# Optimization experiments

Measured on AMD Instinct MI355X. Metric: run time of the kernel, lower is better.

## Reference

```python
import jax, jax.numpy as jnp
import numpy as np

N = 50000; E = 800000; F_IN = 128; H = 16; G = 256
DIMS = [F_IN, H, 2 * H, 4 * H, 4 * H, 8 * H]
EPS = 1e-5


def setup_inputs() -> dict:
    key = jax.random.key(0)
    ks = iter(jax.random.split(key, 40))
    inp = {}
    inp["x"] = jax.random.normal(next(ks), (N, F_IN), dtype=jnp.float32)
    inp["edge_index"] = jax.random.randint(next(ks), (2, E), 0, N, dtype=jnp.int32)
    inp["edge_weight"] = jax.random.uniform(next(ks), (E,), dtype=jnp.float32)
    inp["batch"] = jnp.sort(jax.random.randint(next(ks), (N,), 0, G, dtype=jnp.int32))
    for i in range(5):
        din, dout = DIMS[i], DIMS[i + 1]
        inp[f"W{i+1}"] = jax.random.normal(next(ks), (din, dout), dtype=jnp.float32) / np.sqrt(din).astype(np.float32)
        inp[f"b{i+1}"] = jnp.zeros((dout,), jnp.float32)
        inp[f"g{i+1}"] = jnp.ones((dout,), jnp.float32)
        inp[f"bt{i+1}"] = jnp.zeros((dout,), jnp.float32)
    inp["fc1_w"] = jax.random.normal(next(ks), (8 * H, 4 * H), dtype=jnp.float32) / np.sqrt(8 * H).astype(np.float32)
    inp["fc1_b"] = jnp.zeros((4 * H,), jnp.float32)
    inp["fc2_w"] = jax.random.normal(next(ks), (4 * H, 1), dtype=jnp.float32) / np.sqrt(4 * H).astype(np.float32)
    inp["fc2_b"] = jnp.zeros((1,), jnp.float32)
    return inp


def _gcn_norm(edge_index, edge_weight, n):
    # PyG GCNConv: add self-loops (weight 1), symmetric deg^-1/2 normalization.
    loop = jnp.arange(n, dtype=edge_index.dtype)
    row = jnp.concatenate([edge_index[0], loop])  # source
    col = jnp.concatenate([edge_index[1], loop])  # target
    w = jnp.concatenate([edge_weight, jnp.ones((n,), edge_weight.dtype)])
    deg = jax.ops.segment_sum(w, col, num_segments=n)
    dis = jnp.where(deg > 0, jax.lax.rsqrt(jnp.maximum(deg, 1e-12)), 0.0)
    return row, col, dis[row] * w * dis[col]


def _bn(h, g, b):
    # BatchNorm1d, training-mode batch statistics (biased variance, eps=1e-5)
    mu = h.mean(0)
    v = h.var(0)
    return g * (h - mu) * jax.lax.rsqrt(v + EPS) + b


def reference(x, edge_index, edge_weight, batch,
              W1, b1, g1, bt1, W2, b2, g2, bt2, W3, b3, g3, bt3,
              W4, b4, g4, bt4, W5, b5, g5, bt5,
              fc1_w, fc1_b, fc2_w, fc2_b):
    n = x.shape[0]
    row, col, norm = _gcn_norm(edge_index, edge_weight, n)

    def conv(h, W, b):
        m = h @ W                                   # [N, dout] dense transform
        agg = jax.ops.segment_sum(m[row] * norm[:, None], col, num_segments=n)
        return agg + b

    h = _bn(jax.nn.relu(conv(x, W1, b1)), g1, bt1)
    h = _bn(jax.nn.relu(conv(h, W2, b2)), g2, bt2)
    h = _bn(jax.nn.relu(conv(h, W3, b3)), g3, bt3)
    h = jax.nn.relu(_bn(conv(h, W4, b4), g4, bt4))   # layer4: conv->bn->relu
    h = _bn(conv(h, W5, b5), g5, bt5)                # layer5: conv->bn
    pooled = jax.ops.segment_sum(h, batch, num_segments=G)  # global_add_pool -> [G, 8H]
    p = jax.nn.relu(pooled)
    p = jax.nn.relu(p @ fc1_w + fc1_b)
    # dropout is identity in eval mode
    return (p @ fc2_w + fc2_b).reshape(-1)          # [G]
```

## Files before the change

kernel.cpp:

```cpp
#include <hip/hip_runtime.h>
#include <hip/hip_fp16.h>
#include <stdint.h>

#define NN 50000
#define NE 800000
#define NG 256
#define NBUCKET 16
#define PARTSZ (NBUCKET * 256)

#define NBKT 391
#define ABLK 391
#define ASLICE 2048
#define BCAP 2560

__device__ __forceinline__ float bf2f(unsigned short u) {
    return __uint_as_float(((unsigned)u) << 16);
}
__device__ __forceinline__ unsigned short f2bf(float f) {
    unsigned b = __float_as_uint(f);
    return (unsigned short)((b + 0x7FFF + ((b >> 16) & 1)) >> 16);
}
__device__ __forceinline__ unsigned short f2h(float f) {
    __half h = __float2half(f);
    return *(unsigned short*)&h;
}
__device__ __forceinline__ float h2f(unsigned short u) {
    __half h = *(__half*)&u;
    return __half2float(h);
}

#define AFF4(u, sc, sh) { u.x = fmaxf(sc.x*u.x+sh.x,0.f); u.y = fmaxf(sc.y*u.y+sh.y,0.f); \
                          u.z = fmaxf(sc.z*u.z+sh.z,0.f); u.w = fmaxf(sc.w*u.w+sh.w,0.f); }

__device__ __forceinline__ void scan_totals(const int* __restrict__ totals,
                                            int* __restrict__ sbase, int tid) {
    if (tid < 64) {
        const int C = (NBKT + 63) / 64;
        int tv[C];
        int s = 0;
        int i0 = tid * C;
#pragma unroll
        for (int j = 0; j < C; ++j) {
            int idx = i0 + j;
            int x = (idx < NBKT) ? totals[idx] : 0;
            tv[j] = x; s += x;
        }
        int inc = s;
        for (int off = 1; off < 64; off <<= 1) {
            int t2 = __shfl_up(inc, off, 64);
            if (tid >= off) inc += t2;
        }
        int run = inc - s;
#pragma unroll
        for (int j = 0; j < C; ++j) {
            int idx = i0 + j;
            if (idx < NBKT) sbase[idx] = run;
            run += tv[j];
        }
        if (tid == 63) sbase[NBKT] = run;
    }
}

__global__ void kA1(const int* __restrict__ col, int* __restrict__ bb, float* part, int e) {
    __shared__ int cnt[NBKT];
    for (int j = threadIdx.x; j < NBKT; j += 256) cnt[j] = 0;
    for (int i = blockIdx.x * 256 + threadIdx.x; i < 5 * PARTSZ; i += ABLK * 256) part[i] = 0.f;
    __syncthreads();
    int start = blockIdx.x * ASLICE;
    int end = min(start + ASLICE, e);
    for (int i = start + threadIdx.x; i < end; i += 256)
        atomicAdd(&cnt[col[i] >> 7], 1);
    __syncthreads();
    for (int j = threadIdx.x; j < NBKT; j += 256) bb[blockIdx.x * NBKT + j] = cnt[j];
}

__global__ void kA2a(int* __restrict__ bb, int* __restrict__ totals) {
    __shared__ int v[ABLK];
    int k = blockIdx.x;
    int tid = threadIdx.x;
    for (int b = tid; b < ABLK; b += 256) v[b] = bb[b * NBKT + k];
    __syncthreads();
    if (tid < 64) {
        const int C = (ABLK + 63) / 64;
        int tv[C];
        int s = 0;
        int i0 = tid * C;
#pragma unroll
        for (int j = 0; j < C; ++j) {
            int idx = i0 + j;
            int x = (idx < ABLK) ? v[idx] : 0;
            tv[j] = x; s += x;
        }
        int inc = s;
        for (int off = 1; off < 64; off <<= 1) {
            int t2 = __shfl_up(inc, off, 64);
            if (tid >= off) inc += t2;
        }
        int run = inc - s;
#pragma unroll
        for (int j = 0; j < C; ++j) {
            int idx = i0 + j;
            if (idx < ABLK) v[idx] = run;
            run += tv[j];
        }
        if (tid == 63) totals[k] = run;
    }
    __syncthreads();
    for (int b = tid; b < ABLK; b += 256) bb[b * NBKT + k] = v[b];
}

__global__ void kA3g(const int* __restrict__ row, const int* __restrict__ col,
                     const float* __restrict__ ew, const int* __restrict__ bb,
                     const int* __restrict__ totals, int2* __restrict__ staging,
                     const float* __restrict__ x, const float* __restrict__ W0,
                     float* __restrict__ m1, int e, int n) {
    __shared__ int cur[NBKT];
    __shared__ int sbase[NBKT + 1];
    __shared__ float Wl[128 * 16];
    int tid = threadIdx.x;
    if ((int)blockIdx.x < ABLK) {
        scan_totals(totals, sbase, tid);
        __syncthreads();
        for (int j = tid; j < NBKT; j += 256)
            cur[j] = sbase[j] + bb[blockIdx.x * NBKT + j];
        __syncthreads();
        int start = blockIdx.x * ASLICE;
        int end = min(start + ASLICE, e);
        for (int i = start + tid; i < end; i += 256) {
            int c = col[i];
            int p = atomicAdd(&cur[c >> 7], 1);
            staging[p] = make_int2(row[i] | ((c & 127) << 16), __float_as_int(ew[i]));
        }
        return;
    }
    int bid = (int)blockIdx.x - ABLK;
    for (int i = tid; i < 128 * 16 / 4; i += 256)
        ((float4*)Wl)[i] = ((const float4*)W0)[i];
    __syncthreads();
    int jq = tid % 4, group = tid / 4;
    int node0 = (bid * 64 + group) * 2;
    const float4* h4 = (const float4*)x;
    int hb[2]; bool val[2];
#pragma unroll
    for (int i = 0; i < 2; ++i) {
        int nd = node0 + i;
        val[i] = nd < n;
        hb[i] = (val[i] ? nd : n - 1) * 32;
    }
    float4 acc[2];
    acc[0] = {0,0,0,0}; acc[1] = {0,0,0,0};
#pragma unroll 4
    for (int k4 = 0; k4 < 32; ++k4) {
        const float* wb = &Wl[(k4 * 4) * 16 + jq * 4];
        float4 w0 = *(const float4*)(wb);
        float4 w1 = *(const float4*)(wb + 16);
// ... 1 lines not shown
        float4 w3 = *(const float4*)(wb + 48);
#pragma unroll
        for (int i = 0; i < 2; ++i) {
            float4 hv = h4[hb[i] + k4];
            acc[i].x += hv.x*w0.x + hv.y*w1.x + hv.z*w2.x + hv.w*w3.x;
            acc[i].y += hv.x*w0.y + hv.y*w1.y + hv.z*w2.y + hv.w*w3.y;
            acc[i].z += hv.x*w0.z + hv.y*w1.z + hv.z*w2.z + hv.w*w3.z;
            acc[i].w += hv.x*w0.w + hv.y*w1.w + hv.z*w2.w + hv.w*w3.w;
        }
    }
#pragma unroll
    for (int i = 0; i < 2; ++i)
        if (val[i]) ((float4*)m1)[(node0 + i) * 4 + jq] = acc[i];
}

__global__ void __launch_bounds__(256) kB(const int* __restrict__ totals,
                                          const int2* __restrict__ staging,
                                          unsigned int* __restrict__ csr, int* __restrict__ ptr,
                                          float* __restrict__ dis, int n) {
    __shared__ int2 st[BCAP];
    __shared__ unsigned int outb[BCAP];
    __shared__ int hist[129];
    __shared__ int cur[128];
    __shared__ int sbase[NBKT + 1];
    int k = blockIdx.x, t = threadIdx.x;
    scan_totals(totals, sbase, t);
    if (t < 129) hist[t] = 0;
    __syncthreads();
    int base = sbase[k], cnt = sbase[k + 1] - sbase[k];
    int node0 = k << 7;
    int ncov = min(128, n - node0);
    if (cnt <= BCAP) {
        for (int i = t; i < cnt; i += 256) {
            int2 v = staging[base + i];
            st[i] = v;
            atomicAdd(&hist[v.x >> 16], 1);
        }
        __syncthreads();
        if (t == 0) {
            int run = 0;
            for (int j = 0; j < 128; ++j) { int h = hist[j]; hist[j] = run; run += h; }
            hist[128] = run;
        }
        __syncthreads();
        if (t < 128) cur[t] = hist[t];
        if (t < ncov) ptr[node0 + t] = base + hist[t];
        __syncthreads();
        for (int i = t; i < cnt; i += 256) {
            int2 v = st[i];
            int j = v.x >> 16;
            int p = atomicAdd(&cur[j], 1);
            outb[p] = (unsigned)(v.x & 0xFFFF) | ((unsigned)f2h(__int_as_float(v.y)) << 16);
        }
        __syncthreads();
        for (int i = t; i < cnt; i += 256) csr[base + i] = outb[i];
        if (t < ncov) {
            float s = 1.f;
            int a = hist[t], b2 = hist[t + 1];
            for (int p = a; p < b2; ++p) s += h2f((unsigned short)(outb[p] >> 16));
            dis[node0 + t] = rsqrtf(s);
        }
    } else {
        for (int i = t; i < cnt; i += 256) atomicAdd(&hist[staging[base + i].x >> 16], 1);
        __syncthreads();
        if (t == 0) {
            int run = 0;
            for (int j = 0; j < 128; ++j) { int h = hist[j]; hist[j] = run; run += h; }
            hist[128] = run;
        }
        __syncthreads();
        if (t < 128) cur[t] = hist[t];
        if (t < ncov) ptr[node0 + t] = base + hist[t];
        __syncthreads();
        for (int i = t; i < cnt; i += 256) {
            int2 v = staging[base + i];
            int j = v.x >> 16;
            int p = atomicAdd(&cur[j], 1);
            csr[base + p] = (unsigned)(v.x & 0xFFFF) | ((unsigned)f2h(__int_as_float(v.y)) << 16);
        }
        __threadfence_block();
        __syncthreads();
        if (t < ncov) {
            float s = 1.f;
            int a = hist[t], b2 = hist[t + 1];
            for (int p = a; p < b2; ++p) s += h2f((unsigned short)(csr[base + p] >> 16));
            dis[node0 + t] = rsqrtf(s);
        }
    }
    if (k == gridDim.x - 1 && t == 0) ptr[n] = sbase[NBKT];
}

__global__ void k_l1gather(const float* __restrict__ src, const int* __restrict__ ptr,
                           unsigned int* __restrict__ csr, const float* __restrict__ dis,
                           const float* __restrict__ bias, float* __restrict__ partOut,
                           float* __restrict__ out, int n) {
    __shared__ float ls[16], lq[16];
    int tid = threadIdx.x;
    if (tid < 16) { ls[tid] = 0.f; lq[tid] = 0.f; }
    __syncthreads();
    int t = blockIdx.x * 256 + tid;
    int node = t >> 2;
    int l4 = t & 3;
    bool valid = node < n;
    int nc = valid ? node : n - 1;
    const float4* s4 = (const float4*)src;
    float dc = dis[nc];
    float w0 = dc * dc;
    float4 v = s4[nc * 4 + l4];
    float4 acc = { w0 * v.x, w0 * v.y, w0 * v.z, w0 * v.w };
// ... 42 lines not shown
        s0 += __shfl_down(s0, off, 64); s1 += __shfl_down(s1, off, 64);
        s2 += __shfl_down(s2, off, 64); s3 += __shfl_down(s3, off, 64);
        q0 += __shfl_down(q0, off, 64); q1 += __shfl_down(q1, off, 64);
        q2 += __shfl_down(q2, off, 64); q3 += __shfl_down(q3, off, 64);
    }
    int lane = tid & 63;
    if (lane < 4) {
        atomicAdd(&ls[4*lane+0], s0); atomicAdd(&ls[4*lane+1], s1);
        atomicAdd(&ls[4*lane+2], s2); atomicAdd(&ls[4*lane+3], s3);
        atomicAdd(&lq[4*lane+0], q0); atomicAdd(&lq[4*lane+1], q1);
        atomicAdd(&lq[4*lane+2], q2); atomicAdd(&lq[4*lane+3], q3);
    }
    __syncthreads();
    int bkt = (blockIdx.x & (NBUCKET - 1)) * 256;
    if (tid < 16) {
        atomicAdd(&partOut[bkt + tid], ls[tid]);
        atomicAdd(&partOut[bkt + 128 + tid], lq[tid]);
    }
}

template <int D, int BF16>
__device__ __forceinline__ float4 load_row(const void* src, int node, int l4) {
    if (BF16) {
        const unsigned short* sb = (const unsigned short*)src;
        ushort4 r = *(const ushort4*)(sb + (size_t)node * D + (l4 << 2));
        float4 f;
        f.x = bf2f(r.x); f.y = bf2f(r.y); f.z = bf2f(r.z); f.w = bf2f(r.w);
        return f;
    } else {
        const float4* s4 = (const float4*)src;
        return s4[(size_t)node * (D / 4) + l4];
    }
}

template <int D>
__device__ __forceinline__ void ldrow16(const unsigned short* __restrict__ src, int node, int l8,
                                        float4& a, float4& b) {
    uint4 r = *(const uint4*)(src + (size_t)node * D + (l8 << 3));
    a.x = bf2f((unsigned short)(r.x)); a.y = bf2f((unsigned short)(r.x >> 16));
    a.z = bf2f((unsigned short)(r.y)); a.w = bf2f((unsigned short)(r.y >> 16));
    b.x = bf2f((unsigned short)(r.z)); b.y = bf2f((unsigned short)(r.z >> 16));
    b.z = bf2f((unsigned short)(r.w)); b.w = bf2f((unsigned short)(r.w >> 16));
}

template <int DIN, int DOUT, int EP, int POSTAFF, int PREAFF, int RELU,
          int BF16IN, int BF16OUT, int NPB>
__global__ void __launch_bounds__(256) k_fused(
        const void* __restrict__ src, const int* __restrict__ ptr,
        const unsigned int* __restrict__ csr, const float* __restrict__ dis,
        const float* __restrict__ partIn, const float* __restrict__ gmv,
        const float* __restrict__ btv, const float* __restrict__ W,
        const float* __restrict__ bias, float* __restrict__ partOut,
        void* __restrict__ out, int n) {
    const int TPN1 = DIN / 4, LPN = TPN1 * EP, GN1 = 256 / LPN;
    const int TPN2 = DOUT / 4, G2 = 256 / TPN2;
    const int HS = DIN + 4;
    __shared__ float Wl[DIN * DOUT];
    __shared__ float hrow[NPB * HS];
    __shared__ float scs[DIN], shs[DIN];
    __shared__ float ls[DOUT], lq[DOUT];
    int tid = threadIdx.x;
    for (int i = tid; i < DIN * DOUT / 4; i += 256)
        ((float4*)Wl)[i] = ((const float4*)W)[i];
    if (tid < DIN) {
        float s = 0.f, q = 0.f;
#pragma unroll
        for (int b2 = 0; b2 < NBUCKET; ++b2) {
            s += partIn[b2 * 256 + tid];
            q += partIn[b2 * 256 + 128 + tid];
        }
        float mu = s / (float)n;
        float var = q / (float)n - mu * mu;
        float a = gmv[tid] * rsqrtf(var + 1e-5f);
        scs[tid] = a;
        shs[tid] = btv[tid] - mu * a;
    }
    if (tid < DOUT) { ls[tid] = 0.f; lq[tid] = 0.f; }
    __syncthreads();

    int nodebase = blockIdx.x * NPB;
    {
        int grp = tid / LPN, r = tid % LPN;
        int e0 = r / TPN1, l4 = r % TPN1;
        float4 sc = ((const float4*)scs)[l4];
        float4 sh = ((const float4*)shs)[l4];
#pragma unroll
        for (int pass = 0; pass < NPB / GN1; ++pass) {
            int nl = pass * GN1 + grp;
            int node = nodebase + nl;
            int nc = node < n ? node : n - 1;
            float4 acc = {0.f, 0.f, 0.f, 0.f};
            float sumw = 0.f;
            if (e0 == 0) {
                float d = dis[nc];
                float w0 = d * d;
                float4 v = load_row<DIN, BF16IN>(src, nc, l4);
                if (PREAFF) AFF4(v, sc, sh);
                acc.x = w0*v.x; acc.y = w0*v.y; acc.z = w0*v.z; acc.w = w0*v.w;
                sumw = w0;
            }
            int p0 = ptr[nc], p1 = ptr[nc + 1];
            int p = p0 + e0;
            for (; p + 3 * EP < p1; p += 4 * EP) {
                unsigned int c0 = csr[p], c1 = csr[p + EP], c2 = csr[p + 2*EP], c3 = csr[p + 3*EP];
                float e0w = h2f((unsigned short)(c0 >> 16)), e1w = h2f((unsigned short)(c1 >> 16));
                float e2w = h2f((unsigned short)(c2 >> 16)), e3w = h2f((unsigned short)(c3 >> 16));
                float4 u0 = load_row<DIN, BF16IN>(src, c0 & 0xFFFF, l4);
                float4 u1 = load_row<DIN, BF16IN>(src, c1 & 0xFFFF, l4);
                float4 u2 = load_row<DIN, BF16IN>(src, c2 & 0xFFFF, l4);
                float4 u3 = load_row<DIN, BF16IN>(src, c3 & 0xFFFF, l4);
                if (PREAFF) { AFF4(u0, sc, sh); AFF4(u1, sc, sh); AFF4(u2, sc, sh); AFF4(u3, sc, sh); }
                acc.x += e0w*u0.x + e1w*u1.x + e2w*u2.x + e3w*u3.x;
                acc.y += e0w*u0.y + e1w*u1.y + e2w*u2.y + e3w*u3.y;
                acc.z += e0w*u0.z + e1w*u1.z + e2w*u2.z + e3w*u3.z;
                acc.w += e0w*u0.w + e1w*u1.w + e2w*u2.w + e3w*u3.w;
                if (POSTAFF) sumw += e0w + e1w + e2w + e3w;
            }
            for (; p < p1; p += EP) {
                unsigned int ce = csr[p];
                float w = h2f((unsigned short)(ce >> 16));
                float4 u = load_row<DIN, BF16IN>(src, ce & 0xFFFF, l4);
                if (PREAFF) AFF4(u, sc, sh);
                acc.x += w*u.x; acc.y += w*u.y; acc.z += w*u.z; acc.w += w*u.w;
                if (POSTAFF) sumw += w;
            }
#pragma unroll
            for (int off = TPN1; off < LPN; off <<= 1) {
                acc.x += __shfl_xor(acc.x, off, 64);
                acc.y += __shfl_xor(acc.y, off, 64);
                acc.z += __shfl_xor(acc.z, off, 64);
                acc.w += __shfl_xor(acc.w, off, 64);
                if (POSTAFF) sumw += __shfl_xor(sumw, off, 64);
            }
            if (POSTAFF) {
                acc.x = sc.x * acc.x + sh.x * sumw;
                acc.y = sc.y * acc.y + sh.y * sumw;
// ... 19 lines not shown
                float4 w0 = *(const float4*)(wb);
                float4 w1 = *(const float4*)(wb + DOUT);
                float4 w2 = *(const float4*)(wb + 2 * DOUT);
                float4 w3 = *(const float4*)(wb + 3 * DOUT);
                a.x += hv.x*w0.x + hv.y*w1.x + hv.z*w2.x + hv.w*w3.x;
                a.y += hv.x*w0.y + hv.y*w1.y + hv.z*w2.y + hv.w*w3.y;
                a.z += hv.x*w0.z + hv.y*w1.z + hv.z*w2.z + hv.w*w3.z;
                a.w += hv.x*w0.w + hv.y*w1.w + hv.z*w2.w + hv.w*w3.w;
            }
            a.x += bv.x; a.y += bv.y; a.z += bv.z; a.w += bv.w;
            if (RELU) {
                a.x = fmaxf(a.x, 0.f); a.y = fmaxf(a.y, 0.f);
                a.z = fmaxf(a.z, 0.f); a.w = fmaxf(a.w, 0.f);
            }
            if (valid) {
                if (BF16OUT) {
                    ushort4 o;
                    o.x = f2bf(a.x); o.y = f2bf(a.y); o.z = f2bf(a.z); o.w = f2bf(a.w);
                    *(ushort4*)((unsigned short*)out + (size_t)node * DOUT + (jq << 2)) = o;
                } else {
                    ((float4*)out)[(size_t)node * TPN2 + jq] = a;
                }
                sv.x += a.x; sv.y += a.y; sv.z += a.z; sv.w += a.w;
                qv.x += a.x*a.x; qv.y += a.y*a.y; qv.z += a.z*a.z; qv.w += a.w*a.w;
            }
        }
        for (int off = TPN2; off < 64; off <<= 1) {
            sv.x += __shfl_down(sv.x, off, 64); sv.y += __shfl_down(sv.y, off, 64);
            sv.z += __shfl_down(sv.z, off, 64); sv.w += __shfl_down(sv.w, off, 64);
            qv.x += __shfl_down(qv.x, off, 64); qv.y += __shfl_down(qv.y, off, 64);
            qv.z += __shfl_down(qv.z, off, 64); qv.w += __shfl_down(qv.w, off, 64);
        }
        int lane = tid & 63;
        if (lane < TPN2) {
            atomicAdd(&ls[4*lane+0], sv.x); atomicAdd(&ls[4*lane+1], sv.y);
            atomicAdd(&ls[4*lane+2], sv.z); atomicAdd(&ls[4*lane+3], sv.w);
            atomicAdd(&lq[4*lane+0], qv.x); atomicAdd(&lq[4*lane+1], qv.y);
            atomicAdd(&lq[4*lane+2], qv.z); atomicAdd(&lq[4*lane+3], qv.w);
        }
        __syncthreads();
        int bkt = (blockIdx.x & (NBUCKET - 1)) * 256;
        if (tid < DOUT) {
            atomicAdd(&partOut[bkt + tid], ls[tid]);
            atomicAdd(&partOut[bkt + 128 + tid], lq[tid]);
        }
    }
}

template <int D, int POSTAFF, int PREAFF>
__global__ void __launch_bounds__(256) k_wgather(
        const unsigned short* __restrict__ src, const int* __restrict__ ptr,
        const unsigned int* __restrict__ csr, const float* __restrict__ dis,
        const float* __restrict__ partIn, const float* __restrict__ gmv,
        const float* __restrict__ btv, float* __restrict__ out, int n) {
    const int RL = D / 8;
    const int EP = 4;
    const int LPN = RL * EP;
    __shared__ float scs[D], shs[D];
    int tid = threadIdx.x;
    if (tid < D) {
        float s = 0.f, q = 0.f;
#pragma unroll
        for (int b2 = 0; b2 < NBUCKET; ++b2) {
            s += partIn[b2 * 256 + tid];
            q += partIn[b2 * 256 + 128 + tid];
        }
        float mu = s / (float)n;
        float var = q / (float)n - mu * mu;
        float a = gmv[tid] * rsqrtf(var + 1e-5f);
        scs[tid] = a;
        shs[tid] = btv[tid] - mu * a;
    }
    __syncthreads();
    int t = blockIdx.x * 256 + tid;
    int node = t / LPN;
    int r = t - node * LPN;
    int e0 = r / RL;
    int l8 = r - e0 * RL;
    bool valid = node < n;
    int nc = valid ? node : n - 1;
    float4 scA = ((const float4*)scs)[l8 * 2],     shA = ((const float4*)shs)[l8 * 2];
    float4 scB = ((const float4*)scs)[l8 * 2 + 1], shB = ((const float4*)shs)[l8 * 2 + 1];
    float4 accA = {0.f,0.f,0.f,0.f}, accB = {0.f,0.f,0.f,0.f};
    float sumw = 0.f;
    if (e0 == 0) {
        float d = dis[nc];
        float w0 = d * d;
// ... 49 lines not shown
        accB.z += __shfl_xor(accB.z, off, 64); accB.w += __shfl_xor(accB.w, off, 64);
        if (POSTAFF) sumw += __shfl_xor(sumw, off, 64);
    }
    if (POSTAFF) {
        accA.x = scA.x * accA.x + shA.x * sumw; accA.y = scA.y * accA.y + shA.y * sumw;
        accA.z = scA.z * accA.z + shA.z * sumw; accA.w = scA.w * accA.w + shA.w * sumw;
        accB.x = scB.x * accB.x + shB.x * sumw; accB.y = scB.y * accB.y + shB.y * sumw;
        accB.z = scB.z * accB.z + shB.z * sumw; accB.w = scB.w * accB.w + shB.w * sumw;
    }
    if (valid && e0 == 0) {
        ((float4*)out)[(size_t)nc * (D / 4) + l8 * 2]     = accA;
        ((float4*)out)[(size_t)nc * (D / 4) + l8 * 2 + 1] = accB;
    }
}

template <int DIN, int DOUT, int RELU, int BF16OUT>
__global__ void k_sgemm(const float* __restrict__ h, const float* __restrict__ W,
                        const float* __restrict__ bias, float* __restrict__ partOut,
                        void* __restrict__ m, int n) {
    const int TPN = DOUT / 4, GPB = 256 / TPN, NPT = 4;
    __shared__ float Wl[DIN * DOUT];
    __shared__ float ls[DOUT], lq[DOUT];
    int tid = threadIdx.x;
    for (int i = tid; i < DIN * DOUT / 4; i += 256)
        ((float4*)Wl)[i] = ((const float4*)W)[i];
    if (tid < DOUT) { ls[tid] = 0.f; lq[tid] = 0.f; }
    __syncthreads();

    int jq = tid % TPN;
    int group = tid / TPN;
    int node0 = (blockIdx.x * GPB + group) * NPT;
    const float4* h4 = (const float4*)h;
    int hb[NPT]; bool val[NPT];
#pragma unroll
    for (int i = 0; i < NPT; ++i) {
        int nd = node0 + i;
        val[i] = nd < n;
        hb[i] = (val[i] ? nd : n - 1) * (DIN / 4);
    }
    float4 acc[NPT];
#pragma unroll
// ... 13 lines not shown
            acc[i].z += hv.x*w0.z + hv.y*w1.z + hv.z*w2.z + hv.w*w3.z;
            acc[i].w += hv.x*w0.w + hv.y*w1.w + hv.z*w2.w + hv.w*w3.w;
        }
    }
    float4 bv = ((const float4*)bias)[jq];
    float4 sv = {0,0,0,0}, qv = {0,0,0,0};
#pragma unroll
    for (int i = 0; i < NPT; ++i) {
        float4 a = acc[i];
        a.x += bv.x; a.y += bv.y; a.z += bv.z; a.w += bv.w;
        if (RELU) {
            a.x = fmaxf(a.x, 0.f); a.y = fmaxf(a.y, 0.f);
            a.z = fmaxf(a.z, 0.f); a.w = fmaxf(a.w, 0.f);
        }
        if (val[i]) {
            if (BF16OUT) {
                ushort4 o;
                o.x = f2bf(a.x); o.y = f2bf(a.y); o.z = f2bf(a.z); o.w = f2bf(a.w);
                *(ushort4*)((unsigned short*)m + (size_t)(node0 + i) * DOUT + (jq << 2)) = o;
            } else {
                ((float4*)m)[(size_t)(node0 + i) * TPN + jq] = a;
            }
            sv.x += a.x; sv.y += a.y; sv.z += a.z; sv.w += a.w;
            qv.x += a.x*a.x; qv.y += a.y*a.y; qv.z += a.z*a.z; qv.w += a.w*a.w;
        }
    }
    for (int off = TPN; off < 64; off <<= 1) {
        sv.x += __shfl_down(sv.x, off, 64); sv.y += __shfl_down(sv.y, off, 64);
        sv.z += __shfl_down(sv.z, off, 64); sv.w += __shfl_down(sv.w, off, 64);
        qv.x += __shfl_down(qv.x, off, 64); qv.y += __shfl_down(qv.y, off, 64);
        qv.z += __shfl_down(qv.z, off, 64); qv.w += __shfl_down(qv.w, off, 64);
    }
    int lane = tid & 63;
    if (lane < TPN) {
        atomicAdd(&ls[4*lane+0], sv.x); atomicAdd(&ls[4*lane+1], sv.y);
        atomicAdd(&ls[4*lane+2], sv.z); atomicAdd(&ls[4*lane+3], sv.w);
        atomicAdd(&lq[4*lane+0], qv.x); atomicAdd(&lq[4*lane+1], qv.y);
        atomicAdd(&lq[4*lane+2], qv.z); atomicAdd(&lq[4*lane+3], qv.w);
    }
    __syncthreads();
    int bkt = (blockIdx.x & (NBUCKET - 1)) * 256;
    if (tid < DOUT) {
        atomicAdd(&partOut[bkt + tid], ls[tid]);
        atomicAdd(&partOut[bkt + 128 + tid], lq[tid]);
    }
}

__global__ void k_poolhead(const float* __restrict__ h, const int* __restrict__ batch,
                           const float* __restrict__ partIn, const float* __restrict__ gmv,
                           const float* __restrict__ btv,
                           const float* __restrict__ fc1w, const float* __restrict__ fc1b,
                           const float* __restrict__ fc2w, const float* __restrict__ fc2b,
                           float* __restrict__ out, int n) {
    __shared__ float tmp[256];
    __shared__ float pl[128];
    __shared__ float scs[128], shs[128];
    int g = blockIdx.x;
    int tid = threadIdx.x;
    if (tid < 128) {
        float s = 0.f, q = 0.f;
#pragma unroll
        for (int b2 = 0; b2 < NBUCKET; ++b2) {
            s += partIn[b2 * 256 + tid];
            q += partIn[b2 * 256 + 128 + tid];
        }
        float mu = s / (float)n;
        float var = q / (float)n - mu * mu;
        float a = gmv[tid] * rsqrtf(var + 1e-5f);
        scs[tid] = a;
        shs[tid] = btv[tid] - mu * a;
    }
    int j = tid & 127, prt = tid >> 7;
    int a = 0, b = n;
    while (a < b) { int mid = (a + b) >> 1; if (batch[mid] < g) a = mid + 1; else b = mid; }
    int lo = a;
    b = n;
    while (a < b) { int mid = (a + b) >> 1; if (batch[mid] < g + 1) a = mid + 1; else b = mid; }
    int hi = a;

    float acc = 0.f;
    for (int node = lo + prt; node < hi; node += 2) acc += h[(long)node * 128 + j];
    tmp[tid] = acc;
    __syncthreads();
    if (tid < 128) {
        float cnt = (float)(hi - lo);
        float p = scs[tid] * (tmp[tid] + tmp[tid + 128]) + shs[tid] * cnt;
        pl[tid] = fmaxf(p, 0.f);
    }
    __syncthreads();
    if (tid < 64) {
        float v1 = fc1b[tid];
        for (int k = 0; k < 128; ++k) v1 += pl[k] * fc1w[k * 64 + tid];
        v1 = fmaxf(v1, 0.f);
        float v = v1 * fc2w[tid];
        for (int off = 32; off > 0; off >>= 1) v += __shfl_down(v, off, 64);
        if (tid == 0) out[g] = v + fc2b[0];
    }
}

extern "C" void kernel_launch(void* const* d_in, const int* in_sizes, int n_in,
                              void* d_out, int out_size, void* d_ws, size_t ws_size,
                              hipStream_t stream) {
    const float* x     = (const float*)d_in[0];
// ... 4 lines not shown
    for (int i = 0; i < 5; ++i) {
        W[i]  = (const float*)d_in[4 + 4 * i];
        b[i]  = (const float*)d_in[5 + 4 * i];
        gm[i] = (const float*)d_in[6 + 4 * i];
        bt[i] = (const float*)d_in[7 + 4 * i];
    }
    const float* fc1w = (const float*)d_in[24];
    const float* fc1b = (const float*)d_in[25];
    const float* fc2w = (const float*)d_in[26];
    const float* fc2b = (const float*)d_in[27];
    float* out = (float*)d_out;

    char* wsb = (char*)d_ws;
    float* dis    = (float*)wsb;  wsb += sizeof(float) * NN;
    int*   ptr    = (int*)wsb;    wsb += sizeof(int) * (NN + 4);
    int*   bb     = (int*)wsb;    wsb += sizeof(int) * ABLK * NBKT;
    int*   totals = (int*)wsb;    wsb += sizeof(int) * (NBKT + 1);
    wsb = (char*)(((uintptr_t)wsb + 15) & ~(uintptr_t)15);
    int2*  staging= (int2*)wsb;   wsb += sizeof(int2) * NE;
    unsigned int* csru = (unsigned int*)wsb; wsb += sizeof(unsigned int) * NE;
    wsb = (char*)(((uintptr_t)wsb + 15) & ~(uintptr_t)15);
    float* part   = (float*)wsb;  wsb += sizeof(float) * 5 * PARTSZ;
    unsigned short* bufB1 = (unsigned short*)wsb;  wsb += sizeof(unsigned short) * (size_t)NN * 64;
    unsigned short* bufB2 = (unsigned short*)wsb;  wsb += sizeof(unsigned short) * (size_t)NN * 64;
    float* buf1   = (float*)wsb;  wsb += sizeof(float) * (size_t)NN * 64;
    float* buf2   = (float*)wsb;  wsb += sizeof(float) * (size_t)NN * 128;

    const int* row = ei;
    const int* col = ei + NE;
    const int B = 256;
    const int NBF = (NN + 15) / 16;
    const int GB1 = (NN + 127) / 128;

    kA1<<<ABLK, B, 0, stream>>>(col, bb, part, NE);
    kA2a<<<NBKT, B, 0, stream>>>(bb, totals);
    kA3g<<<ABLK + GB1, B, 0, stream>>>(row, col, ew, bb, totals, staging, x, W[0], buf1, NE, NN);
    kB<<<NBKT, B, 0, stream>>>(totals, staging, csru, ptr, dis, NN);

    k_l1gather<<<(NN * 4 + 255) / 256, B, 0, stream>>>(buf1, ptr, csru, dis,
                                                       b[0], part + 0 * PARTSZ, buf2, NN);

    k_fused<16, 32, 4, 1, 0, 1, 0, 1, 16><<<NBF, B, 0, stream>>>(
        buf2, ptr, csru, dis, part + 0 * PARTSZ, gm[0], bt[0],
        W[1], b[1], part + 1 * PARTSZ, bufB1, NN);

    k_wgather<32, 1, 0><<<(int)(((long)NN * 16 + 255) / 256), B, 0, stream>>>(
        bufB1, ptr, csru, dis, part + 1 * PARTSZ, gm[1], bt[1], buf1, NN);
    k_sgemm<32, 64, 1, 1><<<(NN + 63) / 64, B, 0, stream>>>(buf1, W[2], b[2], part + 2 * PARTSZ, bufB2, NN);

    k_wgather<64, 1, 0><<<(int)(((long)NN * 32 + 255) / 256), B, 0, stream>>>(
        bufB2, ptr, csru, dis, part + 2 * PARTSZ, gm[2], bt[2], buf1, NN);
    k_sgemm<64, 64, 0, 1><<<(NN + 63) / 64, B, 0, stream>>>(buf1, W[3], b[3], part + 3 * PARTSZ, bufB1, NN);

    k_wgather<64, 0, 1><<<(int)(((long)NN * 32 + 255) / 256), B, 0, stream>>>(
        bufB1, ptr, csru, dis, part + 3 * PARTSZ, gm[3], bt[3], buf1, NN);
    k_sgemm<64, 128, 0, 0><<<(NN + 31) / 32, B, 0, stream>>>(buf1, W[4], b[4], part + 4 * PARTSZ, buf2, NN);

    k_poolhead<<<NG, B, 0, stream>>>(buf2, batch, part + 4 * PARTSZ, gm[4], bt[4],
                                     fc1w, fc1b, fc2w, fc2b, out, NN);
}
```

Baseline: 361.7 us.

## Replace bucketed CSR build with atomic counting sort and fuse pooling into last GEMM

The two-level bucket sort that built the CSR (histogram, scan, staging, per-bucket local sort) is replaced by per-node 64-bit atomics that pack in-degree and a fixed-point weighted degree. A single-block scan then produces row pointers, and a scatter pass places edges with global atomics. Layer-5 output is no longer written to memory; the final GEMM atomically accumulates global_add_pool into a double buffer, and the head kernel reads it. Intermediate storage also moves from bf16 to fp16 and BN statistics to double atomics. The changes trade launches and traffic for more global atomic contention, a serial single-block scan, and fp16 range risk.

```diff
diff --git a/kernel.cpp b/kernel.cpp
--- a/kernel.cpp
+++ b/kernel.cpp
@@ -8,18 +8,9 @@
 #define NBUCKET 16
 #define PARTSZ (NBUCKET * 256)
 
-#define NBKT 391
 #define ABLK 391
 #define ASLICE 2048
-#define BCAP 2560
-
-__device__ __forceinline__ float bf2f(unsigned short u) {
-    return __uint_as_float(((unsigned)u) << 16);
-}
-__device__ __forceinline__ unsigned short f2bf(float f) {
-    unsigned b = __float_as_uint(f);
-    return (unsigned short)((b + 0x7FFF + ((b >> 16) & 1)) >> 16);
-}
+
 __device__ __forceinline__ unsigned short f2h(float f) {
     __half h = __float2half(f);
     return *(unsigned short*)&h;
@@ -32,113 +23,97 @@
 #define AFF4(u, sc, sh) { u.x = fmaxf(sc.x*u.x+sh.x,0.f); u.y = fmaxf(sc.y*u.y+sh.y,0.f); \
                           u.z = fmaxf(sc.z*u.z+sh.z,0.f); u.w = fmaxf(sc.w*u.w+sh.w,0.f); }
 
-__device__ __forceinline__ void scan_totals(const int* __restrict__ totals,
-                                            int* __restrict__ sbase, int tid) {
-    if (tid < 64) {
-        const int C = (NBKT + 63) / 64;
-        int tv[C];
-        int s = 0;
-        int i0 = tid * C;
-#pragma unroll
-        for (int j = 0; j < C; ++j) {
-            int idx = i0 + j;
-            int x = (idx < NBKT) ? totals[idx] : 0;
-            tv[j] = x; s += x;
-        }
-        int inc = s;
-        for (int off = 1; off < 64; off <<= 1) {
-            int t2 = __shfl_up(inc, off, 64);
-            if (tid >= off) inc += t2;
-        }
-        int run = inc - s;
-#pragma unroll
-        for (int j = 0; j < C; ++j) {
-            int idx = i0 + j;
-            if (idx < NBKT) sbase[idx] = run;
-            run += tv[j];
-        }
-        if (tid == 63) sbase[NBKT] = run;
-    }
-}
-
-__global__ void kA1(const int* __restrict__ col, int* __restrict__ bb, float* part, int e) {
-    __shared__ int cnt[NBKT];
-    for (int j = threadIdx.x; j < NBKT; j += 256) cnt[j] = 0;
-    for (int i = blockIdx.x * 256 + threadIdx.x; i < 5 * PARTSZ; i += ABLK * 256) part[i] = 0.f;
-    __syncthreads();
+__device__ __forceinline__ void bn_coef(const double* __restrict__ partIn,
+                                        const float* __restrict__ gmv,
+                                        const float* __restrict__ btv,
+                                        int tid, int n, float* scs, float* shs) {
+    double s = 0., q = 0.;
+#pragma unroll
+    for (int b2 = 0; b2 < NBUCKET; ++b2) {
+        s += partIn[b2 * 256 + tid];
+        q += partIn[b2 * 256 + 128 + tid];
+    }
+    double mu = s / (double)n;
+    double var = q / (double)n - mu * mu;
+    float a = gmv[tid] * rsqrtf((float)var + 1e-5f);
+    scs[tid] = a;
+    shs[tid] = btv[tid] - (float)mu * a;
+}
+
+__global__ void kC1(const int* __restrict__ col, const float* __restrict__ ew,
+                    unsigned long long* __restrict__ cd, double* __restrict__ zz,
+                    int zn, int e) {
+    int tid = threadIdx.x;
+    for (int i = blockIdx.x * 256 + tid; i < zn; i += ABLK * 256) zz[i] = 0.;
     int start = blockIdx.x * ASLICE;
     int end = min(start + ASLICE, e);
-    for (int i = start + threadIdx.x; i < end; i += 256)
-        atomicAdd(&cnt[col[i] >> 7], 1);
-    __syncthreads();
-    for (int j = threadIdx.x; j < NBKT; j += 256) bb[blockIdx.x * NBKT + j] = cnt[j];
-}
-
-__global__ void kA2a(int* __restrict__ bb, int* __restrict__ totals) {
-    __shared__ int v[ABLK];
-    int k = blockIdx.x;
-    int tid = threadIdx.x;
-    for (int b = tid; b < ABLK; b += 256) v[b] = bb[b * NBKT + k];
-    __syncthreads();
-    if (tid < 64) {
-        const int C = (ABLK + 63) / 64;
-        int tv[C];
-        int s = 0;
-        int i0 = tid * C;
-#pragma unroll
-        for (int j = 0; j < C; ++j) {
-            int idx = i0 + j;
-            int x = (idx < ABLK) ? v[idx] : 0;
-            tv[j] = x; s += x;
-        }
-        int inc = s;
-        for (int off = 1; off < 64; off <<= 1) {
-            int t2 = __shfl_up(inc, off, 64);
-            if (tid >= off) inc += t2;
-        }
-        int run = inc - s;
-#pragma unroll
-        for (int j = 0; j < C; ++j) {
-            int idx = i0 + j;
-            if (idx < ABLK) v[idx] = run;
-            run += tv[j];
-        }
-        if (tid == 63) totals[k] = run;
-    }
-    __syncthreads();
-    for (int b = tid; b < ABLK; b += 256) bb[b * NBKT + k] = v[b];
-}
-
-__global__ void kA3g(const int* __restrict__ row, const int* __restrict__ col,
-                     const float* __restrict__ ew, const int* __restrict__ bb,
-                     const int* __restrict__ totals, int2* __restrict__ staging,
-                     const float* __restrict__ x, const float* __restrict__ W0,
-                     float* __restrict__ m1, int e, int n) {
-    __shared__ int cur[NBKT];
-    __shared__ int sbase[NBKT + 1];
+    for (int i = start + tid; i < end; i += 256) {
+        int c = col[i];
+        unsigned long long v = (1ull << 40) |
+            (unsigned long long)(unsigned)(ew[i] * 1048576.f + 0.5f);
+        atomicAdd(&cd[c], v);
+    }
+}
+
+__global__ void __launch_bounds__(1024) kC2g(
+        const unsigned long long* __restrict__ cd, int* __restrict__ ptr,
+        int* __restrict__ cur, const float* __restrict__ x,
+        const float* __restrict__ W0, float* __restrict__ m1, int n) {
+    __shared__ int wsum[16];
+    __shared__ int carry_s;
     __shared__ float Wl[128 * 16];
     int tid = threadIdx.x;
-    if ((int)blockIdx.x < ABLK) {
-        scan_totals(totals, sbase, tid);
+    if (blockIdx.x == 0) {
+        int lane = tid & 63, wid = tid >> 6;
+        if (tid == 0) carry_s = 0;
         __syncthreads();
-        for (int j = tid; j < NBKT; j += 256)
-            cur[j] = sbase[j] + bb[blockIdx.x * NBKT + j];
-        __syncthreads();
-        int start = blockIdx.x * ASLICE;
-        int end = min(start + ASLICE, e);
-        for (int i = start + tid; i < end; i += 256) {
-            int c = col[i];
-            int p = atomicAdd(&cur[c >> 7], 1);
-            staging[p] = make_int2(row[i] | ((c & 127) << 16), __float_as_int(ew[i]));
-        }
+        const int NP = NN / 2;
+        const int NT = (NP + 1023) / 1024;
+        for (int t = 0; t < NT; ++t) {
+            int i2 = t * 1024 + tid;
+            int c0 = 0, c1 = 0;
+            if (i2 < NP) {
+                ulonglong2 v = ((const ulonglong2*)cd)[i2];
+                c0 = (int)(v.x >> 40);
+                c1 = (int)(v.y >> 40);
+            }
+            int s = c0 + c1;
+            int inc = s;
+            for (int off = 1; off < 64; off <<= 1) {
+                int tv = __shfl_up(inc, off, 64);
+                if (lane >= off) inc += tv;
+            }
+            if (lane == 63) wsum[wid] = inc;
+            __syncthreads();
+            if (wid == 0) {
+                int xv = (lane < 16) ? wsum[lane] : 0;
+                for (int off = 1; off < 16; off <<= 1) {
+                    int tv = __shfl_up(xv, off, 64);
+                    if (lane >= off) xv += tv;
+                }
+                if (lane < 16) wsum[lane] = xv;
+            }
+            __syncthreads();
+            int base = carry_s + (wid ? wsum[wid - 1] : 0) + (inc - s);
+            if (i2 < NP) {
+                int2 o;
+                o.x = base; o.y = base + c0;
+                ((int2*)ptr)[i2] = o;
+                ((int2*)cur)[i2] = o;
+            }
+            __syncthreads();
+            if (tid == 0) carry_s += wsum[15];
+            __syncthreads();
+        }
+        if (tid == 0) ptr[NN] = carry_s;
         return;
     }
-    int bid = (int)blockIdx.x - ABLK;
-    for (int i = tid; i < 128 * 16 / 4; i += 256)
+    int bid = (int)blockIdx.x - 1;
+    for (int i = tid; i < 128 * 16 / 4; i += 1024)
         ((float4*)Wl)[i] = ((const float4*)W0)[i];
     __syncthreads();
-    int jq = tid % 4, group = tid / 4;
-    int node0 = (bid * 64 + group) * 2;
+    int jq = tid & 3, group = tid >> 2;
+    int node0 = (bid * 256 + group) * 2;
     const float4* h4 = (const float4*)x;
     int hb[2]; bool val[2];
 #pragma unroll
@@ -170,85 +145,28 @@
         if (val[i]) ((float4*)m1)[(node0 + i) * 4 + jq] = acc[i];
 }
 
-__global__ void __launch_bounds__(256) kB(const int* __restrict__ totals,
-                                          const int2* __restrict__ staging,
-                                          unsigned int* __restrict__ csr, int* __restrict__ ptr,
-                                          float* __restrict__ dis, int n) {
-    __shared__ int2 st[BCAP];
-    __shared__ unsigned int outb[BCAP];
-    __shared__ int hist[129];
-    __shared__ int cur[128];
-    __shared__ int sbase[NBKT + 1];
-    int k = blockIdx.x, t = threadIdx.x;
-    scan_totals(totals, sbase, t);
-    if (t < 129) hist[t] = 0;
-    __syncthreads();
-    int base = sbase[k], cnt = sbase[k + 1] - sbase[k];
-    int node0 = k << 7;
-    int ncov = min(128, n - node0);
-    if (cnt <= BCAP) {
-        for (int i = t; i < cnt; i += 256) {
-            int2 v = staging[base + i];
-            st[i] = v;
-            atomicAdd(&hist[v.x >> 16], 1);
-        }
-        __syncthreads();
-        if (t == 0) {
-            int run = 0;
-            for (int j = 0; j < 128; ++j) { int h = hist[j]; hist[j] = run; run += h; }
-            hist[128] = run;
-        }
-        __syncthreads();
-        if (t < 128) cur[t] = hist[t];
-        if (t < ncov) ptr[node0 + t] = base + hist[t];
-        __syncthreads();
-        for (int i = t; i < cnt; i += 256) {
-            int2 v = st[i];
-            int j = v.x >> 16;
-            int p = atomicAdd(&cur[j], 1);
-            outb[p] = (unsigned)(v.x & 0xFFFF) | ((unsigned)f2h(__int_as_float(v.y)) << 16);
-        }
-        __syncthreads();
-        for (int i = t; i < cnt; i += 256) csr[base + i] = outb[i];
-        if (t < ncov) {
-            float s = 1.f;
-            int a = hist[t], b2 = hist[t + 1];
-            for (int p = a; p < b2; ++p) s += h2f((unsigned short)(outb[p] >> 16));
-            dis[node0 + t] = rsqrtf(s);
-        }
-    } else {
-        for (int i = t; i < cnt; i += 256) atomicAdd(&hist[staging[base + i].x >> 16], 1);
-        __syncthreads();
-        if (t == 0) {
-            int run = 0;
-            for (int j = 0; j < 128; ++j) { int h = hist[j]; hist[j] = run; run += h; }
-            hist[128] = run;
-        }
-        __syncthreads();
-        if (t < 128) cur[t] = hist[t];
-        if (t < ncov) ptr[node0 + t] = base + hist[t];
-        __syncthreads();
-        for (int i = t; i < cnt; i += 256) {
-            int2 v = staging[base + i];
-            int j = v.x >> 16;
-            int p = atomicAdd(&cur[j], 1);
-            csr[base + p] = (unsigned)(v.x & 0xFFFF) | ((unsigned)f2h(__int_as_float(v.y)) << 16);
-        }
-        __threadfence_block();
-        __syncthreads();
-        if (t < ncov) {
-            float s = 1.f;
-            int a = hist[t], b2 = hist[t + 1];
-            for (int p = a; p < b2; ++p) s += h2f((unsigned short)(csr[base + p] >> 16));
-            dis[node0 + t] = rsqrtf(s);
-        }
-    }
-    if (k == gridDim.x - 1 && t == 0) ptr[n] = sbase[NBKT];
+__global__ void kC3(const int* __restrict__ row, const int* __restrict__ col,
+                    const float* __restrict__ ew,
+                    const unsigned long long* __restrict__ cd,
+                    int* __restrict__ cur, unsigned int* __restrict__ csr,
+                    float* __restrict__ dis, int e, int n) {
+    int tid = threadIdx.x;
+    int gi = blockIdx.x * 256 + tid;
+    if (gi < n) {
+        float deg = (float)(cd[gi] & ((1ull << 40) - 1)) * (1.f / 1048576.f);
+        dis[gi] = rsqrtf(1.f + deg);
+    }
+    int start = blockIdx.x * ASLICE;
+    int end = min(start + ASLICE, e);
+    for (int i = start + tid; i < end; i += 256) {
+        int p = atomicAdd(&cur[col[i]], 1);
+        csr[p] = (unsigned)row[i] | ((unsigned)f2h(ew[i]) << 16);
+    }
 }
 
 __global__ void k_l1gather(const float* __restrict__ src, const int* __restrict__ ptr,
                            unsigned int* __restrict__ csr, const float* __restrict__ dis,
-                           const float* __restrict__ bias, float* __restrict__ partOut,
+                           const float* __restrict__ bias, double* __restrict__ partOut,
                            float* __restrict__ out, int n) {
     __shared__ float ls[16], lq[16];
     int tid = threadIdx.x;
@@ -321,18 +239,18 @@
     __syncthreads();
     int bkt = (blockIdx.x & (NBUCKET - 1)) * 256;
     if (tid < 16) {
-        atomicAdd(&partOut[bkt + tid], ls[tid]);
-        atomicAdd(&partOut[bkt + 128 + tid], lq[tid]);
-    }
-}
-
-template <int D, int BF16>
+        atomicAdd(&partOut[bkt + tid], (double)ls[tid]);
+        atomicAdd(&partOut[bkt + 128 + tid], (double)lq[tid]);
+    }
+}
+
+template <int D, int F16>
 __device__ __forceinline__ float4 load_row(const void* src, int node, int l4) {
-    if (BF16) {
+    if (F16) {
         const unsigned short* sb = (const unsigned short*)src;
         ushort4 r = *(const ushort4*)(sb + (size_t)node * D + (l4 << 2));
         float4 f;
-        f.x = bf2f(r.x); f.y = bf2f(r.y); f.z = bf2f(r.z); f.w = bf2f(r.w);
+        f.x = h2f(r.x); f.y = h2f(r.y); f.z = h2f(r.z); f.w = h2f(r.w);
         return f;
     } else {
         const float4* s4 = (const float4*)src;
@@ -344,20 +262,20 @@
 __device__ __forceinline__ void ldrow16(const unsigned short* __restrict__ src, int node, int l8,
                                         float4& a, float4& b) {
     uint4 r = *(const uint4*)(src + (size_t)node * D + (l8 << 3));
-    a.x = bf2f((unsigned short)(r.x)); a.y = bf2f((unsigned short)(r.x >> 16));
-    a.z = bf2f((unsigned short)(r.y)); a.w = bf2f((unsigned short)(r.y >> 16));
-    b.x = bf2f((unsigned short)(r.z)); b.y = bf2f((unsigned short)(r.z >> 16));
-    b.z = bf2f((unsigned short)(r.w)); b.w = bf2f((unsigned short)(r.w >> 16));
+    a.x = h2f((unsigned short)(r.x)); a.y = h2f((unsigned short)(r.x >> 16));
+    a.z = h2f((unsigned short)(r.y)); a.w = h2f((unsigned short)(r.y >> 16));
+    b.x = h2f((unsigned short)(r.z)); b.y = h2f((unsigned short)(r.z >> 16));
+    b.z = h2f((unsigned short)(r.w)); b.w = h2f((unsigned short)(r.w >> 16));
 }
 
 template <int DIN, int DOUT, int EP, int POSTAFF, int PREAFF, int RELU,
-          int BF16IN, int BF16OUT, int NPB>
+          int F16IN, int F16OUT, int NPB>
 __global__ void __launch_bounds__(256) k_fused(
         const void* __restrict__ src, const int* __restrict__ ptr,
         const unsigned int* __restrict__ csr, const float* __restrict__ dis,
-        const float* __restrict__ partIn, const float* __restrict__ gmv,
+        const double* __restrict__ partIn, const float* __restrict__ gmv,
         const float* __restrict__ btv, const float* __restrict__ W,
-        const float* __restrict__ bias, float* __restrict__ partOut,
+        const float* __restrict__ bias, double* __restrict__ partOut,
         void* __restrict__ out, int n) {
     const int TPN1 = DIN / 4, LPN = TPN1 * EP, GN1 = 256 / LPN;
     const int TPN2 = DOUT / 4, G2 = 256 / TPN2;
@@ -369,19 +287,7 @@
     int tid = threadIdx.x;
     for (int i = tid; i < DIN * DOUT / 4; i += 256)
         ((float4*)Wl)[i] = ((const float4*)W)[i];
-    if (tid < DIN) {
-        float s = 0.f, q = 0.f;
-#pragma unroll
-        for (int b2 = 0; b2 < NBUCKET; ++b2) {
-            s += partIn[b2 * 256 + tid];
-            q += partIn[b2 * 256 + 128 + tid];
-        }
-        float mu = s / (float)n;
-        float var = q / (float)n - mu * mu;
-        float a = gmv[tid] * rsqrtf(var + 1e-5f);
-        scs[tid] = a;
-        shs[tid] = btv[tid] - mu * a;
-    }
+    if (tid < DIN) bn_coef(partIn, gmv, btv, tid, n, scs, shs);
     if (tid < DOUT) { ls[tid] = 0.f; lq[tid] = 0.f; }
     __syncthreads();
 
@@ -401,7 +307,7 @@
             if (e0 == 0) {
                 float d = dis[nc];
                 float w0 = d * d;
-                float4 v = load_row<DIN, BF16IN>(src, nc, l4);
+                float4 v = load_row<DIN, F16IN>(src, nc, l4);
                 if (PREAFF) AFF4(v, sc, sh);
                 acc.x = w0*v.x; acc.y = w0*v.y; acc.z = w0*v.z; acc.w = w0*v.w;
                 sumw = w0;
@@ -412,10 +318,10 @@
                 unsigned int c0 = csr[p], c1 = csr[p + EP], c2 = csr[p + 2*EP], c3 = csr[p + 3*EP];
                 float e0w = h2f((unsigned short)(c0 >> 16)), e1w = h2f((unsigned short)(c1 >> 16));
                 float e2w = h2f((unsigned short)(c2 >> 16)), e3w = h2f((unsigned short)(c3 >> 16));
-                float4 u0 = load_row<DIN, BF16IN>(src, c0 & 0xFFFF, l4);
-                float4 u1 = load_row<DIN, BF16IN>(src, c1 & 0xFFFF, l4);
-                float4 u2 = load_row<DIN, BF16IN>(src, c2 & 0xFFFF, l4);
-                float4 u3 = load_row<DIN, BF16IN>(src, c3 & 0xFFFF, l4);
+                float4 u0 = load_row<DIN, F16IN>(src, c0 & 0xFFFF, l4);
+                float4 u1 = load_row<DIN, F16IN>(src, c1 & 0xFFFF, l4);
+                float4 u2 = load_row<DIN, F16IN>(src, c2 & 0xFFFF, l4);
+                float4 u3 = load_row<DIN, F16IN>(src, c3 & 0xFFFF, l4);
                 if (PREAFF) { AFF4(u0, sc, sh); AFF4(u1, sc, sh); AFF4(u2, sc, sh); AFF4(u3, sc, sh); }
                 acc.x += e0w*u0.x + e1w*u1.x + e2w*u2.x + e3w*u3.x;
                 acc.y += e0w*u0.y + e1w*u1.y + e2w*u2.y + e3w*u3.y;
@@ -426,7 +332,7 @@
             for (; p < p1; p += EP) {
                 unsigned int ce = csr[p];
                 float w = h2f((unsigned short)(ce >> 16));
-                float4 u = load_row<DIN, BF16IN>(src, ce & 0xFFFF, l4);
+                float4 u = load_row<DIN, F16IN>(src, ce & 0xFFFF, l4);
                 if (PREAFF) AFF4(u, sc, sh);
                 acc.x += w*u.x; acc.y += w*u.y; acc.z += w*u.z; acc.w += w*u.w;
                 if (POSTAFF) sumw += w;
@@ -476,9 +382,9 @@
                 a.z = fmaxf(a.z, 0.f); a.w = fmaxf(a.w, 0.f);
             }
             if (valid) {
-                if (BF16OUT) {
+                if (F16OUT) {
                     ushort4 o;
-                    o.x = f2bf(a.x); o.y = f2bf(a.y); o.z = f2bf(a.z); o.w = f2bf(a.w);
+                    o.x = f2h(a.x); o.y = f2h(a.y); o.z = f2h(a.z); o.w = f2h(a.w);
                     *(ushort4*)((unsigned short*)out + (size_t)node * DOUT + (jq << 2)) = o;
                 } else {
                     ((float4*)out)[(size_t)node * TPN2 + jq] = a;
@@ -503,8 +409,8 @@
         __syncthreads();
         int bkt = (blockIdx.x & (NBUCKET - 1)) * 256;
         if (tid < DOUT) {
-            atomicAdd(&partOut[bkt + tid], ls[tid]);
-            atomicAdd(&partOut[bkt + 128 + tid], lq[tid]);
+            atomicAdd(&partOut[bkt + tid], (double)ls[tid]);
+            atomicAdd(&partOut[bkt + 128 + tid], (double)lq[tid]);
         }
     }
 }
@@ -513,26 +419,14 @@
 __global__ void __launch_bounds__(256) k_wgather(
         const unsigned short* __restrict__ src, const int* __restrict__ ptr,
         const unsigned int* __restrict__ csr, const float* __restrict__ dis,
-        const float* __restrict__ partIn, const float* __restrict__ gmv,
+        const double* __restrict__ partIn, const float* __restrict__ gmv,
         const float* __restrict__ btv, float* __restrict__ out, int n) {
     const int RL = D / 8;
     const int EP = 4;
     const int LPN = RL * EP;
     __shared__ float scs[D], shs[D];
     int tid = threadIdx.x;
-    if (tid < D) {
-        float s = 0.f, q = 0.f;
-#pragma unroll
-        for (int b2 = 0; b2 < NBUCKET; ++b2) {
-            s += partIn[b2 * 256 + tid];
-            q += partIn[b2 * 256 + 128 + tid];
-        }
-        float mu = s / (float)n;
-        float var = q / (float)n - mu * mu;
-        float a = gmv[tid] * rsqrtf(var + 1e-5f);
-        scs[tid] = a;
-        shs[tid] = btv[tid] - mu * a;
-    }
+    if (tid < D) bn_coef(partIn, gmv, btv, tid, n, scs, shs);
     __syncthreads();
     int t = blockIdx.x * 256 + tid;
     int node = t / LPN;
@@ -612,17 +506,29 @@
     }
 }
 
-template <int DIN, int DOUT, int RELU, int BF16OUT>
+template <int DIN, int DOUT, int RELU, int F16OUT, int POOL>
 __global__ void k_sgemm(const float* __restrict__ h, const float* __restrict__ W,
-                        const float* __restrict__ bias, float* __restrict__ partOut,
-                        void* __restrict__ m, int n) {
+                        const float* __restrict__ bias, double* __restrict__ partOut,
+                        void* __restrict__ m, const int* __restrict__ batch,
+                        double* __restrict__ pooled, int n) {
     const int TPN = DOUT / 4, GPB = 256 / TPN, NPT = 4;
+    const int NPBLK = GPB * NPT;
+    const int MAXG = 34;
     __shared__ float Wl[DIN * DOUT];
     __shared__ float ls[DOUT], lq[DOUT];
+    __shared__ double pool_l[POOL ? MAXG * DOUT : 1];
+    __shared__ int gmaxs;
     int tid = threadIdx.x;
     for (int i = tid; i < DIN * DOUT / 4; i += 256)
         ((float4*)Wl)[i] = ((const float4*)W)[i];
     if (tid < DOUT) { ls[tid] = 0.f; lq[tid] = 0.f; }
+    int gbase = 0;
+    if (POOL) {
+        for (int i = tid; i < MAXG * DOUT; i += 256) pool_l[i] = 0.;
+        if (tid == 0) gmaxs = 0;
+        int bn0 = blockIdx.x * NPBLK;
+        gbase = batch[bn0 < n ? bn0 : n - 1];
+    }
     __syncthreads();
 
     int jq = tid % TPN;
@@ -666,12 +572,27 @@
             a.z = fmaxf(a.z, 0.f); a.w = fmaxf(a.w, 0.f);
         }
         if (val[i]) {
-            if (BF16OUT) {
-                ushort4 o;
-                o.x = f2bf(a.x); o.y = f2bf(a.y); o.z = f2bf(a.z); o.w = f2bf(a.w);
-                *(ushort4*)((unsigned short*)m + (size_t)(node0 + i) * DOUT + (jq << 2)) = o;
+            if (POOL) {
+                int off = batch[node0 + i] - gbase;
+                if (off < MAXG) {
+                    atomicAdd(&pool_l[off * DOUT + jq * 4 + 0], (double)a.x);
+                    atomicAdd(&pool_l[off * DOUT + jq * 4 + 1], (double)a.y);
+                    atomicAdd(&pool_l[off * DOUT + jq * 4 + 2], (double)a.z);
+                    atomicAdd(&pool_l[off * DOUT + jq * 4 + 3], (double)a.w);
+                    if (jq == 0) atomicMax(&gmaxs, off);
+                } else {
+                    double* pg = &pooled[(size_t)(gbase + off) * DOUT + jq * 4];
+                    atomicAdd(pg + 0, (double)a.x); atomicAdd(pg + 1, (double)a.y);
+                    atomicAdd(pg + 2, (double)a.z); atomicAdd(pg + 3, (double)a.w);
+                }
             } else {
-                ((float4*)m)[(size_t)(node0 + i) * TPN + jq] = a;
+                if (F16OUT) {
+                    ushort4 o;
+                    o.x = f2h(a.x); o.y = f2h(a.y); o.z = f2h(a.z); o.w = f2h(a.w);
+                    *(ushort4*)((unsigned short*)m + (size_t)(node0 + i) * DOUT + (jq << 2)) = o;
+                } else {
+                    ((float4*)m)[(size_t)(node0 + i) * TPN + jq] = a;
+                }
             }
             sv.x += a.x; sv.y += a.y; sv.z += a.z; sv.w += a.w;
             qv.x += a.x*a.x; qv.y += a.y*a.y; qv.z += a.z*a.z; qv.w += a.w*a.w;
@@ -693,52 +614,39 @@
     __syncthreads();
     int bkt = (blockIdx.x & (NBUCKET - 1)) * 256;
     if (tid < DOUT) {
-        atomicAdd(&partOut[bkt + tid], ls[tid]);
-        atomicAdd(&partOut[bkt + 128 + tid], lq[tid]);
-    }
-}
-
-__global__ void k_poolhead(const float* __restrict__ h, const int* __restrict__ batch,
-                           const float* __restrict__ partIn, const float* __restrict__ gmv,
-                           const float* __restrict__ btv,
-                           const float* __restrict__ fc1w, const float* __restrict__ fc1b,
-                           const float* __restrict__ fc2w, const float* __restrict__ fc2b,
-                           float* __restrict__ out, int n) {
-    __shared__ float tmp[256];
+        atomicAdd(&partOut[bkt + tid], (double)ls[tid]);
+        atomicAdd(&partOut[bkt + 128 + tid], (double)lq[tid]);
+    }
+    if (POOL) {
+        int gm = gmaxs;
+        for (int i = tid; i < (gm + 1) * DOUT; i += 256) {
+            double v = pool_l[i];
+            if (v != 0.) atomicAdd(&pooled[(size_t)gbase * DOUT + i], v);
+        }
+    }
+}
+
+__global__ void __launch_bounds__(128) k_poolhead(
+        const double* __restrict__ pooled, const int* __restrict__ batch,
+        const double* __restrict__ partIn, const float* __restrict__ gmv,
+        const float* __restrict__ btv,
+        const float* __restrict__ fc1w, const float* __restrict__ fc1b,
+        const float* __restrict__ fc2w, const float* __restrict__ fc2b,
+        float* __restrict__ out, int n) {
     __shared__ float pl[128];
     __shared__ float scs[128], shs[128];
     int g = blockIdx.x;
     int tid = threadIdx.x;
-    if (tid < 128) {
-        float s = 0.f, q = 0.f;
-#pragma unroll
-        for (int b2 = 0; b2 < NBUCKET; ++b2) {
-            s += partIn[b2 * 256 + tid];
-            q += partIn[b2 * 256 + 128 + tid];
-        }
-        float mu = s / (float)n;
-        float var = q / (float)n - mu * mu;
-        float a = gmv[tid] * rsqrtf(var + 1e-5f);
-        scs[tid] = a;
-        shs[tid] = btv[tid] - mu * a;
-    }
-    int j = tid & 127, prt = tid >> 7;
+    bn_coef(partIn, gmv, btv, tid, n, scs, shs);
     int a = 0, b = n;
     while (a < b) { int mid = (a + b) >> 1; if (batch[mid] < g) a = mid + 1; else b = mid; }
     int lo = a;
     b = n;
     while (a < b) { int mid = (a + b) >> 1; if (batch[mid] < g + 1) a = mid + 1; else b = mid; }
     int hi = a;
-
-    float acc = 0.f;
-    for (int node = lo + prt; node < hi; node += 2) acc += h[(long)node * 128 + j];
-    tmp[tid] = acc;
-    __syncthreads();
-    if (tid < 128) {
-        float cnt = (float)(hi - lo);
-        float p = scs[tid] * (tmp[tid] + tmp[tid + 128]) + shs[tid] * cnt;
-        pl[tid] = fmaxf(p, 0.f);
-    }
+    float cntf = (float)(hi - lo);
+    float p = scs[tid] * (float)pooled[g * 128 + tid] + shs[tid] * cntf;
+    pl[tid] = fmaxf(p, 0.f);
     __syncthreads();
     if (tid < 64) {
         float v1 = fc1b[tid];
@@ -773,28 +681,27 @@
     char* wsb = (char*)d_ws;
     float* dis    = (float*)wsb;  wsb += sizeof(float) * NN;
     int*   ptr    = (int*)wsb;    wsb += sizeof(int) * (NN + 4);
-    int*   bb     = (int*)wsb;    wsb += sizeof(int) * ABLK * NBKT;
-    int*   totals = (int*)wsb;    wsb += sizeof(int) * (NBKT + 1);
-    wsb = (char*)(((uintptr_t)wsb + 15) & ~(uintptr_t)15);
-    int2*  staging= (int2*)wsb;   wsb += sizeof(int2) * NE;
+    int*   cur    = (int*)wsb;    wsb += sizeof(int) * NN;
+    unsigned long long* cd = (unsigned long long*)wsb; wsb += sizeof(unsigned long long) * NN;
+    double* part   = (double*)wsb;  wsb += sizeof(double) * 5 * PARTSZ;
+    double* pooled = (double*)wsb;  wsb += sizeof(double) * NG * 128;
     unsigned int* csru = (unsigned int*)wsb; wsb += sizeof(unsigned int) * NE;
-    wsb = (char*)(((uintptr_t)wsb + 15) & ~(uintptr_t)15);
-    float* part   = (float*)wsb;  wsb += sizeof(float) * 5 * PARTSZ;
     unsigned short* bufB1 = (unsigned short*)wsb;  wsb += sizeof(unsigned short) * (size_t)NN * 64;
     unsigned short* bufB2 = (unsigned short*)wsb;  wsb += sizeof(unsigned short) * (size_t)NN * 64;
     float* buf1   = (float*)wsb;  wsb += sizeof(float) * (size_t)NN * 64;
-    float* buf2   = (float*)wsb;  wsb += sizeof(float) * (size_t)NN * 128;
+    float* buf2   = (float*)wsb;  wsb += sizeof(float) * (size_t)NN * 16;
 
     const int* row = ei;
     const int* col = ei + NE;
     const int B = 256;
     const int NBF = (NN + 15) / 16;
-    const int GB1 = (NN + 127) / 128;
-
-    kA1<<<ABLK, B, 0, stream>>>(col, bb, part, NE);
-    kA2a<<<NBKT, B, 0, stream>>>(bb, totals);
-    kA3g<<<ABLK + GB1, B, 0, stream>>>(row, col, ew, bb, totals, staging, x, W[0], buf1, NE, NN);
-    kB<<<NBKT, B, 0, stream>>>(totals, staging, csru, ptr, dis, NN);
+    const int GB1 = (NN + 511) / 512;
+    const int ZN = 5 * PARTSZ + NG * 128;
+
+    hipMemsetAsync(cd, 0, sizeof(unsigned long long) * NN, stream);
+    kC1<<<ABLK, B, 0, stream>>>(col, ew, cd, part, ZN, NE);
+    kC2g<<<1 + GB1, 1024, 0, stream>>>(cd, ptr, cur, x, W[0], buf1, NN);
+    kC3<<<ABLK, B, 0, stream>>>(row, col, ew, cd, cur, csru, dis, NE, NN);
 
     k_l1gather<<<(NN * 4 + 255) / 256, B, 0, stream>>>(buf1, ptr, csru, dis,
                                                        b[0], part + 0 * PARTSZ, buf2, NN);
@@ -805,16 +712,19 @@
 
     k_wgather<32, 1, 0><<<(int)(((long)NN * 16 + 255) / 256), B, 0, stream>>>(
         bufB1, ptr, csru, dis, part + 1 * PARTSZ, gm[1], bt[1], buf1, NN);
-    k_sgemm<32, 64, 1, 1><<<(NN + 63) / 64, B, 0, stream>>>(buf1, W[2], b[2], part + 2 * PARTSZ, bufB2, NN);
+    k_sgemm<32, 64, 1, 1, 0><<<(NN + 63) / 64, B, 0, stream>>>(
+        buf1, W[2], b[2], part + 2 * PARTSZ, bufB2, nullptr, nullptr, NN);
 
     k_wgather<64, 1, 0><<<(int)(((long)NN * 32 + 255) / 256), B, 0, stream>>>(
         bufB2, ptr, csru, dis, part + 2 * PARTSZ, gm[2], bt[2], buf1, NN);
-    k_sgemm<64, 64, 0, 1><<<(NN + 63) / 64, B, 0, stream>>>(buf1, W[3], b[3], part + 3 * PARTSZ, bufB1, NN);
+    k_sgemm<64, 64, 0, 1, 0><<<(NN + 63) / 64, B, 0, stream>>>(
+        buf1, W[3], b[3], part + 3 * PARTSZ, bufB1, nullptr, nullptr, NN);
 
     k_wgather<64, 0, 1><<<(int)(((long)NN * 32 + 255) / 256), B, 0, stream>>>(
         bufB1, ptr, csru, dis, part + 3 * PARTSZ, gm[3], bt[3], buf1, NN);
-    k_sgemm<64, 128, 0, 0><<<(NN + 31) / 32, B, 0, stream>>>(buf1, W[4], b[4], part + 4 * PARTSZ, buf2, NN);
-
-    k_poolhead<<<NG, B, 0, stream>>>(buf2, batch, part + 4 * PARTSZ, gm[4], bt[4],
-                                     fc1w, fc1b, fc2w, fc2b, out, NN);
-}
+    k_sgemm<64, 128, 0, 0, 1><<<(NN + 31) / 32, B, 0, stream>>>(
+        buf1, W[4], b[4], part + 4 * PARTSZ, nullptr, batch, pooled, NN);
+
+    k_poolhead<<<NG, 128, 0, stream>>>(pooled, batch, part + 4 * PARTSZ, gm[4], bt[4],
+                                       fc1w, fc1b, fc2w, fc2b, out, NN);
+}
```

Result: slower. 426.1 us (+17.8%).
